# Performance work log

Measured on AMD Instinct MI355X. Metric: run time of the kernel, lower is better.

Reference implementation:

```python
import jax, jax.numpy as jnp
import numpy as np

N_NODES = 100000
N_EDGES = 1600000
D_IN = 128
D_OUT = 128
BN_EPS = 1e-5


def setup_inputs() -> dict:
    key = jax.random.key(0)
    ks = jax.random.split(key, 6)
    x = jax.random.normal(ks[0], (N_NODES, D_IN), dtype=jnp.float32)
    edge_index = jax.random.randint(ks[1], (2, N_EDGES), 0, N_NODES, dtype=jnp.int32)
    edge_weight = jax.random.uniform(ks[2], (N_EDGES,), dtype=jnp.float32)
    W = jax.random.normal(ks[3], (D_IN, D_OUT), dtype=jnp.float32) / np.sqrt(D_IN)
    b = jax.random.normal(ks[4], (D_OUT,), dtype=jnp.float32) * 0.01
    gamma = jnp.ones((D_OUT,), dtype=jnp.float32)
    beta = jnp.zeros((D_OUT,), dtype=jnp.float32)
    return {"x": x, "edge_index": edge_index, "edge_weight": edge_weight,
            "W": W, "b": b, "gamma": gamma, "beta": beta}


def reference(x, edge_index, edge_weight, W, b, gamma, beta):
    n = x.shape[0]
    # add self loops (add_self_loops=True)
    self_loops = jnp.arange(n, dtype=edge_index.dtype)
    row = jnp.concatenate([edge_index[0], self_loops])  # source
    col = jnp.concatenate([edge_index[1], self_loops])  # destination
    ew = jnp.concatenate([edge_weight, jnp.ones((n,), x.dtype)])
    # degree via scatter-add of ones on source nodes
    deg = jax.ops.segment_sum(jnp.ones_like(ew), row, num_segments=n)
    dinv = jnp.where(deg > 0, jax.lax.rsqrt(deg), 0.0)
    norm = dinv[row] * dinv[col] * ew  # [E+N]
    # linear transform
    h = x @ W + b  # [N, D_OUT]
    # per-edge gather -> scale -> scatter-add (vectorized form of the python loop)
    msgs = norm[:, None] * h[row]  # [E+N, D_OUT]
    out = jax.ops.segment_sum(msgs, col, num_segments=n)  # [N, D_OUT]
    # BatchNorm1d (training mode: biased batch stats)
    mean = jnp.mean(out, axis=0)
    var = jnp.mean(jnp.square(out - mean), axis=0)
    out = (out - mean) * jax.lax.rsqrt(var + BN_EPS) * gamma + beta
    return jax.nn.relu(out)
```

## Files before the change

kernel.cpp:

```cpp
#include <hip/hip_runtime.h>

#define DD 128
#define BINCAP 4608
#define S1_EPB 7168
#define DEG_R 16384
#define DEG_S 8

typedef __attribute__((ext_vector_type(8))) short short8;
typedef __attribute__((ext_vector_type(4))) float f32x4;

__device__ __forceinline__ unsigned short f2bf(float f) {
    unsigned int u; __builtin_memcpy(&u, &f, 4);
    unsigned int r = (u + 0x7FFFu + ((u >> 16) & 1u)) >> 16;
    return (unsigned short)r;
}
__device__ __forceinline__ unsigned int pack_bf(float a, float b) {
    return (unsigned int)f2bf(a) | ((unsigned int)f2bf(b) << 16);
}
__device__ __forceinline__ float lo_bf(unsigned int p) {
    unsigned int u = (p & 0xFFFFu) << 16; float f; __builtin_memcpy(&f, &u, 4); return f;
}
__device__ __forceinline__ float hi_bf(unsigned int p) {
    unsigned int u = p & 0xFFFF0000u; float f; __builtin_memcpy(&f, &u, 4); return f;
}
__device__ __forceinline__ float i2f(int v) { float f; __builtin_memcpy(&f, &v, 4); return f; }
__device__ __forceinline__ int f2i(float v) { int i; __builtin_memcpy(&i, &v, 4); return i; }

__global__ void k_prep(int* deg, int* cursor, float* colsumR, float* colsumsqR, int N, int NBIN,
                       int nInit, const float* __restrict__ W, unsigned short* __restrict__ Wfrag) {
    int bid = blockIdx.x, t = threadIdx.x;
    if (bid < nInit) {
        int i = bid * 256 + t;
        if (i < N) deg[i] = 1;
        if (i < NBIN) cursor[i] = 0;
        if (i < 1024) { colsumR[i] = 0.0f; colsumsqR[i] = 0.0f; }
        return;
    }
    int i = (bid - nInit) * 256 + t;
    int k = i >> 7, n = i & 127;
    int tt = n >> 4, s = k >> 5, l = (((k >> 3) & 3) << 4) | (n & 15), j = k & 7;
    Wfrag[((tt * 4 + s) * 64 + l) * 8 + j] = f2bf(W[k * DD + n]);
}

__global__ __launch_bounds__(1024) void k_fused(
    const int* __restrict__ ei, const float* __restrict__ ew,
    int* __restrict__ deg, int* __restrict__ cursor, long long* __restrict__ coarse,
    int E, int N, int NBIN, int nS1i, int nDeg,
    const float* __restrict__ x, const unsigned short* __restrict__ Wfrag,
    const float* __restrict__ b, unsigned short* __restrict__ h)
{
    __shared__ int smem[16384];
    int t = threadIdx.x;
    int id = blockIdx.x;
    int role, rid;
    if (id < 2 * nS1i)           { role = (id & 1); rid = id >> 1; }
    else if (id < 2 * nS1i + nDeg) { role = 2; rid = id - 2 * nS1i; }
    else                         { role = 1; rid = nS1i + (id - 2 * nS1i - nDeg); }

    const int* row = ei;
    const int* col = ei + E;

    if (role == 0) {
        int* scnt  = smem;
        int* soff  = smem + 512;
        int* gbase = smem + 1024;
        long long* sorted = (long long*)(smem + 1536);
        for (int i = t; i < 512; i += 1024) scnt[i] = 0;
        __syncthreads();
        int e0 = rid * S1_EPB;
        int myrank[7];
#pragma unroll
        for (int j = 0; j < 7; ++j) {
            int e = e0 + j * 1024 + t;
            if (e < E) myrank[j] = atomicAdd(&scnt[col[e] >> 8], 1);
        }
        __syncthreads();
        if (t < 512) soff[t] = scnt[t];
        __syncthreads();
        for (int off = 1; off < 512; off <<= 1) {
            int v = 0;
            if (t < 512 && t >= off) v = soff[t - off];
            __syncthreads();
            if (t < 512) soff[t] += v;
            __syncthreads();
        }
        if (t < NBIN && scnt[t] > 0) gbase[t] = atomicAdd(&cursor[t], scnt[t]);
#pragma unroll
        for (int j = 0; j < 7; ++j) {
            int e = e0 + j * 1024 + t;
            if (e < E) {
                int c = col[e];
                int bn = c >> 8;
                int lo = row[e] | ((c & 255) << 17);
                long long ent = ((long long)(unsigned)f2i(ew[e]) << 32) | (unsigned)lo;
                sorted[(soff[bn] - scnt[bn]) + myrank[j]] = ent;
            }
        }
        __syncthreads();
        int wave = t >> 6, lane = t & 63;
        for (int bn = wave; bn < NBIN; bn += 16) {
            int k = scnt[bn];
            if (k == 0) continue;
            int off0 = soff[bn] - k;
            int gb = gbase[bn];
            long long* dst = coarse + (size_t)bn * BINCAP;
            for (int j = lane; j < k; j += 64) {
                int gp = gb + j;
                if (gp < BINCAP) dst[gp] = sorted[off0 + j];
            }
        }
        return;
    }
    if (role == 2) {
        int nr = (N + DEG_R - 1) / DEG_R;
        int ri = rid % nr, si = rid / nr;
        int* lc = smem;
        for (int i = t; i < DEG_R; i += 1024) lc[i] = 0;
        __syncthreads();
        int base = ri * DEG_R;
        int per = (E + DEG_S - 1) / DEG_S;
        int es = si * per, ee = es + per; if (ee > E) ee = E;
        int q0 = es >> 2, q1 = ee >> 2;
        const int4* r4 = (const int4*)row;
        for (int q = q0 + t; q < q1; q += 1024) {
            int4 v = r4[q];
            unsigned d0 = (unsigned)(v.x - base), d1 = (unsigned)(v.y - base);
            unsigned d2 = (unsigned)(v.z - base), d3 = (unsigned)(v.w - base);
            if (d0 < DEG_R) atomicAdd(&lc[d0], 1);
            if (d1 < DEG_R) atomicAdd(&lc[d1], 1);
            if (d2 < DEG_R) atomicAdd(&lc[d2], 1);
            if (d3 < DEG_R) atomicAdd(&lc[d3], 1);
        }
        for (int e = (q1 << 2) + t; e < ee; e += 1024) {
            unsigned d = (unsigned)(row[e] - base);
            if (d < DEG_R) atomicAdd(&lc[d], 1);
        }
        __syncthreads();
        for (int i = t; i < DEG_R; i += 1024) {
            int node = base + i, k = lc[i];
            if (node < N && k) atomicAdd(&deg[node], k);
        }
        return;
    }
    int lane = t & 63, wave = t >> 6;
    int row0 = rid * 256 + wave * 16;
    int mrow = row0 + (lane & 15);
    int kgrp = lane >> 4;
    f32x4 acc[8];
#pragma unroll
    for (int i = 0; i < 8; ++i) acc[i] = (f32x4){0.f, 0.f, 0.f, 0.f};
    const short8* Wf = (const short8*)Wfrag;
#pragma unroll
    for (int s = 0; s < 4; ++s) {
        float xv[8];
        if (mrow < N) {
            const float4* xp = (const float4*)(x + (size_t)mrow * DD + s * 32 + kgrp * 8);
            float4 xa = xp[0], xb = xp[1];
            xv[0] = xa.x; xv[1] = xa.y; xv[2] = xa.z; xv[3] = xa.w;
            xv[4] = xb.x; xv[5] = xb.y; xv[6] = xb.z; xv[7] = xb.w;
        } else {
#pragma unroll
            for (int j = 0; j < 8; ++j) xv[j] = 0.f;
        }
        short8 af;
#pragma unroll
        for (int j = 0; j < 8; ++j) af[j] = (short)f2bf(xv[j]);
#pragma unroll
        for (int tt = 0; tt < 8; ++tt) {
            short8 bf = Wf[(tt * 4 + s) * 64 + lane];
            acc[tt] = __builtin_amdgcn_mfma_f32_16x16x32_bf16(af, bf, acc[tt], 0, 0, 0);
        }
    }
    int drow = row0 + (lane >> 4) * 4;
    int coll = lane & 15;
#pragma unroll
    for (int tt = 0; tt < 8; ++tt) {
        int cc = tt * 16 + coll;
        float bias = b[cc];
#pragma unroll
        for (int rr = 0; rr < 4; ++rr) {
            int rw = drow + rr;
            if (rw < N) h[(size_t)rw * DD + cc] = f2bf(acc[tt][rr] + bias);
        }
    }
}

__global__ __launch_bounds__(1024) void k_agg(
    const long long* __restrict__ coarse, const int* __restrict__ cursor,
    const int* __restrict__ deg, const unsigned int* __restrict__ h,
    unsigned int* __restrict__ outb, float* __restrict__ colsumR,
    float* __restrict__ colsumsqR, int N)
{
    __shared__ long long sorted2[BINCAP];
    __shared__ int fcnt[256], fpos[256], fcur[256];
    __shared__ float ls[2048], lq[2048];
    int bn = blockIdx.x, t = threadIdx.x;
    int m = cursor[bn]; if (m > BINCAP) m = BINCAP;
    for (int i = t; i < 256; i += 1024) fcnt[i] = 0;
    __syncthreads();
    const long long* src = coarse + (size_t)bn * BINCAP;
    for (int i = t; i < m; i += 1024) {
        int lo = (int)src[i];
        atomicAdd(&fcnt[(lo >> 17) & 255], 1);
    }
    __syncthreads();
    if (t < 256) fpos[t] = fcnt[t];
    __syncthreads();
    for (int off = 1; off < 256; off <<= 1) {
        int v = 0;
        if (t < 256 && t >= off) v = fpos[t - off];
        __syncthreads();
        if (t < 256) fpos[t] += v;
        __syncthreads();
    }
    if (t < 256) fcur[t] = fpos[t] - fcnt[t];
    __syncthreads();
    for (int i = t; i < m; i += 1024) {
        long long v = src[i];
        int lo = (int)v;
        int clo = (lo >> 17) & 255;
        int sr = lo & 0x1FFFF;
        int c = (bn << 8) + clo;
        float w = rsqrtf((float)deg[sr]) * rsqrtf((float)deg[c]) * i2f((int)(v >> 32));
        int p = atomicAdd(&fcur[clo], 1);
        sorted2[p] = ((long long)(unsigned)f2i(w) << 32) | (unsigned)sr;
    }
    __syncthreads();
    int wave = t >> 6, lane = t & 63;
    float s0 = 0, s1 = 0, q0 = 0, q1 = 0;
    const int2* sp = (const int2*)sorted2;
    for (int d = wave; d < 256; d += 16) {
        int c = (bn << 8) + d;
        if (c >= N) continue;
        float dn = rsqrtf((float)deg[c]);
        float sn = dn * dn;
        unsigned int p = h[(size_t)c * 64 + lane];
        float a0 = sn * lo_bf(p), a1 = sn * hi_bf(p);
        int cn = fcnt[d];
        int off0 = fpos[d] - cn;
        int j = 0;
        for (; j + 8 <= cn; j += 8) {
            int2 d0 = sp[off0 + j],     d1 = sp[off0 + j + 1];
            int2 d2 = sp[off0 + j + 2], d3 = sp[off0 + j + 3];
            int2 d4 = sp[off0 + j + 4], d5 = sp[off0 + j + 5];
            int2 d6 = sp[off0 + j + 6], d7 = sp[off0 + j + 7];
            unsigned int g0 = h[(size_t)d0.x * 64 + lane];
            unsigned int g1 = h[(size_t)d1.x * 64 + lane];
            unsigned int g2 = h[(size_t)d2.x * 64 + lane];
            unsigned int g3 = h[(size_t)d3.x * 64 + lane];
            unsigned int g4 = h[(size_t)d4.x * 64 + lane];
            unsigned int g5 = h[(size_t)d5.x * 64 + lane];
            unsigned int g6 = h[(size_t)d6.x * 64 + lane];
            unsigned int g7 = h[(size_t)d7.x * 64 + lane];
            float w0 = i2f(d0.y), w1 = i2f(d1.y), w2 = i2f(d2.y), w3 = i2f(d3.y);
            float w4 = i2f(d4.y), w5 = i2f(d5.y), w6 = i2f(d6.y), w7 = i2f(d7.y);
            a0 = fmaf(w0, lo_bf(g0), a0); a1 = fmaf(w0, hi_bf(g0), a1);
            a0 = fmaf(w1, lo_bf(g1), a0); a1 = fmaf(w1, hi_bf(g1), a1);
            a0 = fmaf(w2, lo_bf(g2), a0); a1 = fmaf(w2, hi_bf(g2), a1);
            a0 = fmaf(w3, lo_bf(g3), a0); a1 = fmaf(w3, hi_bf(g3), a1);
            a0 = fmaf(w4, lo_bf(g4), a0); a1 = fmaf(w4, hi_bf(g4), a1);
            a0 = fmaf(w5, lo_bf(g5), a0); a1 = fmaf(w5, hi_bf(g5), a1);
            a0 = fmaf(w6, lo_bf(g6), a0); a1 = fmaf(w6, hi_bf(g6), a1);
            a0 = fmaf(w7, lo_bf(g7), a0); a1 = fmaf(w7, hi_bf(g7), a1);
        }
        for (; j < cn; ++j) {
            int2 dd = sp[off0 + j];
            unsigned int g = h[(size_t)dd.x * 64 + lane];
            float w = i2f(dd.y);
            a0 = fmaf(w, lo_bf(g), a0);
            a1 = fmaf(w, hi_bf(g), a1);
        }
        outb[(size_t)c * 64 + lane] = pack_bf(a0, a1);
        s0 += a0; q0 += a0 * a0;
        s1 += a1; q1 += a1 * a1;
    }
    ls[wave * 128 + lane * 2] = s0; ls[wave * 128 + lane * 2 + 1] = s1;
    lq[wave * 128 + lane * 2] = q0; lq[wave * 128 + lane * 2 + 1] = q1;
    __syncthreads();
    if (t < 128) {
        float S = 0, Q = 0;
#pragma unroll
        for (int w = 0; w < 16; ++w) { S += ls[w * 128 + t]; Q += lq[w * 128 + t]; }
        int rep = (bn & 7) * 128 + t;
        atomicAdd(&colsumR[rep], S);
        atomicAdd(&colsumsqR[rep], Q);
    }
}

__global__ __launch_bounds__(256) void k_bn(
    const unsigned int* __restrict__ outb, float* __restrict__ out,
    const float* __restrict__ colsumR, const float* __restrict__ colsumsqR,
    const float* __restrict__ gamma, const float* __restrict__ beta,
    int N, int total64)
{
    __shared__ float ss[256];
    int t = threadIdx.x;
    if (t < 128) {
        float S = 0, Q = 0;
#pragma unroll
        for (int r = 0; r < 8; ++r) { S += colsumR[r * 128 + t]; Q += colsumsqR[r * 128 + t]; }
        float invN = 1.0f / (float)N;
        float mean = S * invN;
        float var = Q * invN - mean * mean;
        float inv = rsqrtf(var + 1e-5f);
        float sc = gamma[t] * inv;
        ss[t] = sc;
        ss[128 + t] = beta[t] - mean * sc;
    }
    __syncthreads();
    for (int i = blockIdx.x * 256 + t; i < total64; i += gridDim.x * 256) {
        int c0 = (i & 63) * 2;
        unsigned int p = outb[i];
        float v0 = fmaxf(lo_bf(p) * ss[c0]     + ss[128 + c0],     0.0f);
        float v1 = fmaxf(hi_bf(p) * ss[c0 + 1] + ss[128 + c0 + 1], 0.0f);
        ((float2*)out)[i] = make_float2(v0, v1);
    }
}

extern "C" void kernel_launch(void* const* d_in, const int* in_sizes, int n_in,
                              void* d_out, int out_size, void* d_ws, size_t ws_size,
                              hipStream_t stream) {
    const float* x     = (const float*)d_in[0];
    const int* ei      = (const int*)d_in[1];
    const float* ew    = (const float*)d_in[2];
    const float* W     = (const float*)d_in[3];
    const float* b     = (const float*)d_in[4];
    const float* gamma = (const float*)d_in[5];
    const float* beta  = (const float*)d_in[6];
    float* out = (float*)d_out;

    int N = in_sizes[0] / DD;
    int E = in_sizes[2];
    int NBIN = (N + 255) / 256;

    char* wsb = (char*)d_ws;
    size_t off = 0;
    auto alloc = [&](size_t bytes) -> char* {
        char* p = wsb + off;
        off = (off + bytes + 255) & ~(size_t)255;
        return p;
    };
    int* deg        = (int*)alloc((size_t)N * 4);
    int* cursor     = (int*)alloc((size_t)NBIN * 4);
    long long* coarse = (long long*)alloc((size_t)NBIN * BINCAP * 8);
    unsigned short* h = (unsigned short*)alloc((size_t)N * DD * 2);
    unsigned short* Wfrag = (unsigned short*)alloc(DD * DD * 2);
    unsigned int* outb = (unsigned int*)alloc((size_t)N * 64 * 4);
    float* colsumR   = (float*)alloc(1024 * 4);
    float* colsumsqR = (float*)alloc(1024 * 4);

    int nInit = (N + 255) / 256;
    int nS1   = (E + S1_EPB - 1) / S1_EPB;
    int nGemm = (N + 255) / 256;
    int nS1i  = (nS1 < nGemm) ? nS1 : nGemm;
    int nDeg  = ((N + DEG_R - 1) / DEG_R) * DEG_S;
    int GF    = 2 * nS1i + nDeg + (nGemm - nS1i);

    k_prep<<<dim3(nInit + 64), dim3(256), 0, stream>>>(deg, cursor, colsumR, colsumsqR,
                                                       N, NBIN, nInit, W, Wfrag);
    k_fused<<<dim3(GF), dim3(1024), 0, stream>>>(ei, ew, deg, cursor, coarse, E, N, NBIN,
                                                 nS1i, nDeg, x, Wfrag, b, h);
    k_agg<<<dim3(NBIN), dim3(1024), 0, stream>>>(coarse, cursor, deg, (const unsigned int*)h,
                                                 outb, colsumR, colsumsqR, N);
    k_bn<<<dim3(2048), dim3(256), 0, stream>>>(outb, out, colsumR, colsumsqR,
                                               gamma, beta, N, N * 64);
}
```

Measured before the change: 236.7 us.

## Sub-bucket edges by source range so aggregation sweeps h in source-sorted phases

In the aggregation kernel, edges in each destination bin are now bucketed by destination and by the source-node range (sr>>14, giving 7 tiles). Each wave keeps 16 destination accumulators in registers and walks all of them for each source tile in turn, so concurrent gathers from h stay within a narrower source window. The goal is better L2/cache locality on the random h gathers. The cost is a 1024-wide scan in place of a 256-wide one, more register pressure, and shorter inner loops unrolled only by 2, which lowers memory-level parallelism.

```diff
diff --git a/kernel.cpp b/kernel.cpp
--- a/kernel.cpp
+++ b/kernel.cpp
@@ -5,6 +5,7 @@
 #define S1_EPB 7168
 #define DEG_R 16384
 #define DEG_S 8
+#define NT 7
 
 typedef __attribute__((ext_vector_type(8))) short short8;
 typedef __attribute__((ext_vector_type(4))) float f32x4;
@@ -192,87 +193,91 @@
     float* __restrict__ colsumsqR, int N)
 {
     __shared__ long long sorted2[BINCAP];
-    __shared__ int fcnt[256], fpos[256], fcur[256];
-    __shared__ float ls[2048], lq[2048];
+    __shared__ int fpos[2048], fcur[2048];
     int bn = blockIdx.x, t = threadIdx.x;
     int m = cursor[bn]; if (m > BINCAP) m = BINCAP;
-    for (int i = t; i < 256; i += 1024) fcnt[i] = 0;
+    for (int i = t; i < 2048; i += 1024) fcur[i] = 0;
     __syncthreads();
     const long long* src = coarse + (size_t)bn * BINCAP;
     for (int i = t; i < m; i += 1024) {
         int lo = (int)src[i];
-        atomicAdd(&fcnt[(lo >> 17) & 255], 1);
-    }
-    __syncthreads();
-    if (t < 256) fpos[t] = fcnt[t];
-    __syncthreads();
-    for (int off = 1; off < 256; off <<= 1) {
-        int v = 0;
-        if (t < 256 && t >= off) v = fpos[t - off];
-        __syncthreads();
-        if (t < 256) fpos[t] += v;
-        __syncthreads();
-    }
-    if (t < 256) fcur[t] = fpos[t] - fcnt[t];
+        int key = (((lo >> 17) & 255) << 3) | ((lo & 0x1FFFF) >> 14);
+        atomicAdd(&fcur[key], 1);
+    }
+    __syncthreads();
+    int v0 = fcur[2 * t], v1 = fcur[2 * t + 1];
+    int sthis = v0 + v1;
+    int* scratch = (int*)sorted2;
+    scratch[t] = sthis;
+    __syncthreads();
+    for (int off = 1; off < 1024; off <<= 1) {
+        int vv = (t >= off) ? scratch[t - off] : 0;
+        __syncthreads();
+        scratch[t] += vv;
+        __syncthreads();
+    }
+    int excl = scratch[t] - sthis;
+    fpos[2 * t] = excl;       fcur[2 * t] = excl;
+    fpos[2 * t + 1] = excl + v0; fcur[2 * t + 1] = excl + v0;
     __syncthreads();
     for (int i = t; i < m; i += 1024) {
         long long v = src[i];
         int lo = (int)v;
-        int clo = (lo >> 17) & 255;
+        int dlow = (lo >> 17) & 255;
         int sr = lo & 0x1FFFF;
-        int c = (bn << 8) + clo;
+        int c = (bn << 8) + dlow;
         float w = rsqrtf((float)deg[sr]) * rsqrtf((float)deg[c]) * i2f((int)(v >> 32));
-        int p = atomicAdd(&fcur[clo], 1);
+        int p = atomicAdd(&fcur[(dlow << 3) | (sr >> 14)], 1);
         sorted2[p] = ((long long)(unsigned)f2i(w) << 32) | (unsigned)sr;
     }
     __syncthreads();
     int wave = t >> 6, lane = t & 63;
+    float aL[16], aH[16];
+#pragma unroll
+    for (int i = 0; i < 16; ++i) {
+        int c = (bn << 8) + wave + 16 * i;
+        if (c < N) {
+            float dn = rsqrtf((float)deg[c]);
+            float sn = dn * dn;
+            unsigned int p = h[(size_t)c * 64 + lane];
+            aL[i] = sn * lo_bf(p); aH[i] = sn * hi_bf(p);
+        } else { aL[i] = 0.f; aH[i] = 0.f; }
+    }
+    const int2* sp = (const int2*)sorted2;
+    for (int T = 0; T < NT; ++T) {
+#pragma unroll
+        for (int i = 0; i < 16; ++i) {
+            int d = wave + 16 * i;
+            int k = (d << 3) | T;
+            int j = fpos[k], j1 = fcur[k];
+            for (; j + 2 <= j1; j += 2) {
+                int2 e0 = sp[j], e1 = sp[j + 1];
+                unsigned int g0 = h[(size_t)e0.x * 64 + lane];
+                unsigned int g1 = h[(size_t)e1.x * 64 + lane];
+                float w0 = i2f(e0.y), w1 = i2f(e1.y);
+                aL[i] = fmaf(w0, lo_bf(g0), aL[i]); aH[i] = fmaf(w0, hi_bf(g0), aH[i]);
+                aL[i] = fmaf(w1, lo_bf(g1), aL[i]); aH[i] = fmaf(w1, hi_bf(g1), aH[i]);
+            }
+            if (j < j1) {
+                int2 e = sp[j];
+                unsigned int g = h[(size_t)e.x * 64 + lane];
+                float w = i2f(e.y);
+                aL[i] = fmaf(w, lo_bf(g), aL[i]); aH[i] = fmaf(w, hi_bf(g), aH[i]);
+            }
+        }
+    }
+    __syncthreads();
+    float* ls = (float*)sorted2;
+    float* lq = ls + 2048;
     float s0 = 0, s1 = 0, q0 = 0, q1 = 0;
-    const int2* sp = (const int2*)sorted2;
-    for (int d = wave; d < 256; d += 16) {
-        int c = (bn << 8) + d;
-        if (c >= N) continue;
-        float dn = rsqrtf((float)deg[c]);
-        float sn = dn * dn;
-        unsigned int p = h[(size_t)c * 64 + lane];
-        float a0 = sn * lo_bf(p), a1 = sn * hi_bf(p);
-        int cn = fcnt[d];
-        int off0 = fpos[d] - cn;
-        int j = 0;
-        for (; j + 8 <= cn; j += 8) {
-            int2 d0 = sp[off0 + j],     d1 = sp[off0 + j + 1];
-            int2 d2 = sp[off0 + j + 2], d3 = sp[off0 + j + 3];
-            int2 d4 = sp[off0 + j + 4], d5 = sp[off0 + j + 5];
-            int2 d6 = sp[off0 + j + 6], d7 = sp[off0 + j + 7];
-            unsigned int g0 = h[(size_t)d0.x * 64 + lane];
-            unsigned int g1 = h[(size_t)d1.x * 64 + lane];
-            unsigned int g2 = h[(size_t)d2.x * 64 + lane];
-            unsigned int g3 = h[(size_t)d3.x * 64 + lane];
-            unsigned int g4 = h[(size_t)d4.x * 64 + lane];
-            unsigned int g5 = h[(size_t)d5.x * 64 + lane];
-            unsigned int g6 = h[(size_t)d6.x * 64 + lane];
-            unsigned int g7 = h[(size_t)d7.x * 64 + lane];
-            float w0 = i2f(d0.y), w1 = i2f(d1.y), w2 = i2f(d2.y), w3 = i2f(d3.y);
-            float w4 = i2f(d4.y), w5 = i2f(d5.y), w6 = i2f(d6.y), w7 = i2f(d7.y);
-            a0 = fmaf(w0, lo_bf(g0), a0); a1 = fmaf(w0, hi_bf(g0), a1);
-            a0 = fmaf(w1, lo_bf(g1), a0); a1 = fmaf(w1, hi_bf(g1), a1);
-            a0 = fmaf(w2, lo_bf(g2), a0); a1 = fmaf(w2, hi_bf(g2), a1);
-            a0 = fmaf(w3, lo_bf(g3), a0); a1 = fmaf(w3, hi_bf(g3), a1);
-            a0 = fmaf(w4, lo_bf(g4), a0); a1 = fmaf(w4, hi_bf(g4), a1);
-            a0 = fmaf(w5, lo_bf(g5), a0); a1 = fmaf(w5, hi_bf(g5), a1);
-            a0 = fmaf(w6, lo_bf(g6), a0); a1 = fmaf(w6, hi_bf(g6), a1);
-            a0 = fmaf(w7, lo_bf(g7), a0); a1 = fmaf(w7, hi_bf(g7), a1);
-        }
-        for (; j < cn; ++j) {
-            int2 dd = sp[off0 + j];
-            unsigned int g = h[(size_t)dd.x * 64 + lane];
-            float w = i2f(dd.y);
-            a0 = fmaf(w, lo_bf(g), a0);
-            a1 = fmaf(w, hi_bf(g), a1);
-        }
-        outb[(size_t)c * 64 + lane] = pack_bf(a0, a1);
-        s0 += a0; q0 += a0 * a0;
-        s1 += a1; q1 += a1 * a1;
+#pragma unroll
+    for (int i = 0; i < 16; ++i) {
+        int c = (bn << 8) + wave + 16 * i;
+        if (c < N) {
+            outb[(size_t)c * 64 + lane] = pack_bf(aL[i], aH[i]);
+            s0 += aL[i]; q0 += aL[i] * aL[i];
+            s1 += aH[i]; q1 += aH[i] * aH[i];
+        }
     }
     ls[wave * 128 + lane * 2] = s0; ls[wave * 128 + lane * 2 + 1] = s1;
     lq[wave * 128 + lane * 2] = q0; lq[wave * 128 + lane * 2 + 1] = q1;
```

Result: slower. 320.7 us (+35.5%).
